# Performance work log

Hardware: AMD Instinct MI355X
Metric: run time of the kernel (lower is better)

The kernel has to match this reference:

```python
import jax, jax.numpy as jnp
import numpy as np

EMBED_DIM = 1024
HEADS = 16
HEAD_DIM = EMBED_DIM // HEADS
ROPE_THETA = 10000.0


def apply_rope(x):
    # x: [B, H, T, D]; standard rotary embedding on head_dim, half-split style
    D = x.shape[-1]
    T = x.shape[-2]
    half = D // 2
    inv_freq = 1.0 / (ROPE_THETA ** (jnp.arange(half, dtype=jnp.float32) / half))
    ang = jnp.arange(T, dtype=jnp.float32)[:, None] * inv_freq[None, :]  # [T, half]
    cos, sin = jnp.cos(ang), jnp.sin(ang)  # [T, half]
    x1, x2 = x[..., :half], x[..., half:]
    return jnp.concatenate([x1 * cos - x2 * sin, x1 * sin + x2 * cos], axis=-1)


def setup_inputs() -> dict:
    key = jax.random.key(0)
    ks = jax.random.split(key, 6)
    B, T, E, H = 2, 2048, EMBED_DIM, HEADS
    s = 0.02
    return {
        "x": jax.random.normal(ks[0], (B, T, E), dtype=jnp.float32),
        "w_qkv": jax.random.normal(ks[1], (E, 3 * E), dtype=jnp.float32) * s,
        "w_pre": jax.random.normal(ks[2], (H, H), dtype=jnp.float32) * s,
        "w_post": jax.random.normal(ks[3], (H, H), dtype=jnp.float32) * s,
        "w_out": jax.random.normal(ks[4], (E, E), dtype=jnp.float32) * s,
        "b_out": jax.random.normal(ks[5], (E,), dtype=jnp.float32) * s,
    }


def reference(x, w_qkv, w_pre, w_post, w_out, b_out):
    B, T, E = x.shape
    H, D = HEADS, HEAD_DIM
    qkv = x @ w_qkv  # [B, T, 3E]
    q, k, v = jnp.split(qkv, 3, axis=-1)
    q = q.reshape(B, T, H, D).transpose(0, 2, 1, 3)  # [B,H,T,D]
    k = k.reshape(B, T, H, D).transpose(0, 2, 1, 3)
    v = v.reshape(B, T, H, D).transpose(0, 2, 1, 3)
    q = apply_rope(q)
    k = apply_rope(k)
    scale = D ** -0.5
    dots = jnp.einsum('bhid,bhjd->bhij', q, k) * scale  # [B,H,T,T]
    # pre-softmax talking-heads mixing: new_head g = sum_h w_pre[g,h] * dots[h]
    dots = jnp.einsum('bhij,gh->bgij', dots, w_pre)
    attn = jax.nn.softmax(dots, axis=-1)
    # post-softmax mixing
    attn = jnp.einsum('bhij,gh->bgij', attn, w_post)
    out = jnp.einsum('bhij,bhjd->bhid', attn, v)  # [B,H,T,D]
    out = out.transpose(0, 2, 1, 3).reshape(B, T, E)
    return out @ w_out.T + b_out  # dropout is identity in eval
```

## Files before the change

### kernel.cpp

```cpp
#include <hip/hip_runtime.h>
#include <stdint.h>

typedef unsigned short u16;
typedef unsigned int   u32;

#define T_SEQ 2048
#define NB 2
#define NH 16
#define HD 64
#define E_DIM 1024
#define E3 3072
#define JS1 4
#define JS2 4
#define S2 36
#define OS2 1040

typedef float f32x4 __attribute__((ext_vector_type(4)));
typedef short s16x8 __attribute__((ext_vector_type(8)));

__device__ __forceinline__ float b2f(u16 u) {
    union { float f; u32 i; } v; v.i = ((u32)u) << 16; return v.f;
}
__device__ __forceinline__ u16 f2b(float f) {
    union { float f; u32 i; } v; v.f = f;
    u32 x = v.i;
    return (u16)((x + 0x7FFFu + ((x >> 16) & 1u)) >> 16);
}
__device__ __forceinline__ f32x4 mfma_bf16(s16x8 a, s16x8 b, f32x4 c) {
    return __builtin_amdgcn_mfma_f32_16x16x32_bf16(a, b, c, 0, 0, 0);
}
__device__ __forceinline__ void gl_lds16(const void* g, void* l) {
    __builtin_amdgcn_global_load_lds((const __attribute__((address_space(1))) void*)g,
                                     (__attribute__((address_space(3))) void*)l, 16, 0, 0);
}

__global__ void k_detect(const u16* __restrict__ x, int* __restrict__ flag) {
    __shared__ int cnt[256];
    int tid = threadIdx.x;
    int insane = 0;
    for (int i = tid; i < 4096; i += 256) {
        u16 v = x[2 * i];
        int e = (v >> 7) & 0xFF;
        if (e >= 143 || (e > 0 && e <= 100)) insane++;
    }
    cnt[tid] = insane;
    __syncthreads();
    if (tid == 0) {
        int s = 0;
        for (int k = 0; k < 256; ++k) s += cnt[k];
        *flag = (s > 512) ? 1 : 0;
    }
}

__global__ void k_cvt_bf16(const void* __restrict__ src, u16* __restrict__ dst,
                           int n, const int* __restrict__ flag) {
    int i = blockIdx.x * 256 + threadIdx.x;
    bool f32 = (*flag) != 0;
    if (i < n) dst[i] = f32 ? f2b(((const float*)src)[i]) : ((const u16*)src)[i];
}

__global__ void k_cvt_small(const void* __restrict__ a, const void* __restrict__ b,
                            const void* __restrict__ c, float* __restrict__ da,
                            float* __restrict__ db, float* __restrict__ dc,
                            const int* __restrict__ flag) {
    int i = blockIdx.x * 256 + threadIdx.x;
    bool f32 = (*flag) != 0;
    if (i < 256) {
        da[i] = f32 ? ((const float*)a)[i] : b2f(((const u16*)a)[i]);
    } else if (i < 512) {
        int j = i - 256;
        db[j] = f32 ? ((const float*)b)[j] : b2f(((const u16*)b)[j]);
    } else if (i < 1536) {
        int j = i - 512;
        dc[j] = f32 ? ((const float*)c)[j] : b2f(((const u16*)c)[j]);
    }
}

__global__ void k_zero(uint4* p, int n16) {
    int i = blockIdx.x * 256 + threadIdx.x;
    if (i < n16) p[i] = uint4{0u, 0u, 0u, 0u};
}

__global__ void k_transpose(const void* __restrict__ w, u16* __restrict__ wT,
                            const int* __restrict__ flag) {
    __shared__ u16 tile[32][33];
    bool f32 = (*flag) != 0;
    int n0 = blockIdx.x * 32;
    int k0 = blockIdx.y * 32;
    int tid = threadIdx.x;
    int c = tid & 31, r4 = tid >> 5;
#pragma unroll
    for (int it = 0; it < 4; ++it) {
        int r = r4 + it * 8;
        size_t idx = (size_t)(k0 + r) * E3 + n0 + c;
        tile[r][c] = f32 ? f2b(((const float*)w)[idx]) : ((const u16*)w)[idx];
    }
    __syncthreads();
#pragma unroll
    for (int it = 0; it < 4; ++it) {
        int r = r4 + it * 8;
        wT[(size_t)(n0 + r) * E_DIM + k0 + c] = tile[c][r];
    }
}

__global__ void k_qkv(const u16* __restrict__ A, const u16* __restrict__ Bm,
                      u16* __restrict__ C) {
    __shared__ __align__(16) u16 As[128 * 32];
    __shared__ __align__(16) u16 Bs[128 * 32];
    int m0 = blockIdx.x * 128, n0 = blockIdx.y * 128;
    int tid = threadIdx.x, lane = tid & 63, wv = tid >> 6;
    int q = lane >> 4, l = lane & 15;
    int wm = (wv >> 1) * 64, wn = (wv & 1) * 64;
    f32x4 acc[4][4] = {};
    int r16 = lane >> 2;
    int ccol = (lane & 3) * 8;
    for (int kc = 0; kc < 1024; kc += 32) {
#pragma unroll
        for (int j = 0; j < 4; ++j) {
            int chunk = wv * 4 + j;
            if (chunk < 8) {
                const u16* g = A + (size_t)(m0 + chunk * 16 + r16) * 1024 + kc + ccol;
                gl_lds16(g, (char*)As + chunk * 1024);
            } else {
                int ch = chunk - 8;
                const u16* g = Bm + (size_t)(n0 + ch * 16 + r16) * 1024 + kc + ccol;
                gl_lds16(g, (char*)Bs + ch * 1024);
            }
        }
        __syncthreads();
        s16x8 af[4], bf[4];
#pragma unroll
        for (int t = 0; t < 4; ++t) {
            af[t] = *(const s16x8*)(As + (wm + t * 16 + l) * 32 + q * 8);
            bf[t] = *(const s16x8*)(Bs + (wn + t * 16 + l) * 32 + q * 8);
        }
#pragma unroll
        for (int i = 0; i < 4; ++i)
#pragma unroll
            for (int j2 = 0; j2 < 4; ++j2)
                acc[i][j2] = mfma_bf16(af[i], bf[j2], acc[i][j2]);
        __syncthreads();
    }
#pragma unroll
    for (int i = 0; i < 4; ++i)
#pragma unroll
        for (int j2 = 0; j2 < 4; ++j2)
#pragma unroll
            for (int r = 0; r < 4; ++r) {
                int row = m0 + wm + i * 16 + q * 4 + r;
                int col = n0 + wn + j2 * 16 + l;
                C[(size_t)row * E3 + col] = f2b(acc[i][j2][r]);
            }
}

__global__ void k_rope(const u16* __restrict__ qkv, u16* __restrict__ qr,
                       u16* __restrict__ kr, u16* __restrict__ vt) {
    __shared__ u16 tile[64][66];
    int t0 = blockIdx.x * 64;
    int h = blockIdx.y, b = blockIdx.z;
    int tid = threadIdx.x;
    const float LN_TH = 9.210340371976184f / 32.0f;
    for (int src = 0; src < 3; ++src) {
        {
            int d = tid & 63, tr = tid >> 6;
#pragma unroll
            for (int it = 0; it < 16; ++it) {
                int t = tr + it * 4;
                tile[t][d] = qkv[(size_t)(b * T_SEQ + t0 + t) * E3 + src * E_DIM + h * HD + d];
            }
        }
        __syncthreads();
        if (src < 2) {
            u16* dst = (src == 0 ? qr : kr) + ((size_t)(b * NH + h) * T_SEQ) * HD;
            int d = tid & 31, tr = tid >> 5;
            float inv = __expf(-(float)d * LN_TH);
#pragma unroll
            for (int it = 0; it < 8; ++it) {
                int t = tr + it * 8;
                float ang = (float)(t0 + t) * inv;
                float sn, cs;
                __sincosf(ang, &sn, &cs);
                float x1 = b2f(tile[t][d]);
                float x2 = b2f(tile[t][d + 32]);
                dst[(size_t)(t0 + t) * HD + d]      = f2b(x1 * cs - x2 * sn);
                dst[(size_t)(t0 + t) * HD + d + 32] = f2b(x1 * sn + x2 * cs);
            }
        } else {
            int tl = tid & 63, dr = tid >> 6;
#pragma unroll
            for (int it = 0; it < 16; ++it) {
                int d = dr + it * 4;
                vt[((size_t)(b * NH + h) * HD + d) * T_SEQ + t0 + tl] = tile[tl][d];
            }
        }
        __syncthreads();
    }
}

__global__ __launch_bounds__(256, 3) void k_pass1(const u16* __restrict__ qr, const u16* __restrict__ kr,
                                                  const float* __restrict__ w_pre, float* __restrict__ lsum) {
    __shared__ __align__(16) u16 dots[256 * S2];
    int lin = blockIdx.x;
    int combo = lin & 7;
    int b = combo >> 2, js = combo & 3;
    int i0 = (lin >> 3) * 32;
    int tid = threadIdx.x, lane = tid & 63, wv = tid >> 6;
    int q = lane >> 4, l = lane & 15;
    {
        uint2* p = (uint2*)(dots + tid * S2 + 16);
        uint2 z = {0u, 0u};
        p[0] = z; p[1] = z; p[2] = z; p[3] = z;
    }
    s16x8 wpre;
#pragma unroll
    for (int jj = 0; jj < 8; ++jj) {
        int hh = q * 8 + jj;
        wpre[jj] = (hh < 16) ? (short)f2b(w_pre[l * 16 + hh] * 0.125f) : (short)0;
    }
    s16x8 qf[2][4][2];
#pragma unroll
    for (int it = 0; it < 2; ++it)
#pragma unroll
        for (int hl = 0; hl < 4; ++hl) {
            int h = wv * 4 + hl;
            const u16* ptr = qr + ((size_t)(b * NH + h) * T_SEQ + i0 + it * 16 + l) * HD + q * 8;
            qf[it][hl][0] = *(const s16x8*)(ptr);
            qf[it][hl][1] = *(const s16x8*)(ptr + 32);
        }
    float lacc[2][4][4] = {};
    __syncthreads();
    int jbase = js * (T_SEQ / JS1);
    for (int jstep = 0; jstep < (T_SEQ / JS1) / 16; ++jstep) {
        int jh = jbase + jstep * 16;
        s16x8 kf[4][2];
#pragma unroll
        for (int hl = 0; hl < 4; ++hl) {
            int h = wv * 4 + hl;
            const u16* ptr = kr + ((size_t)(b * NH + h) * T_SEQ + jh + l) * HD + q * 8;
            kf[hl][0] = *(const s16x8*)(ptr);
            kf[hl][1] = *(const s16x8*)(ptr + 32);
        }
#pragma unroll
        for (int it = 0; it < 2; ++it) {
            f32x4 dacc[4];
#pragma unroll
            for (int hl = 0; hl < 4; ++hl) {
                f32x4 z = {};
                z = mfma_bf16(qf[it][hl][0], kf[hl][0], z);
                z = mfma_bf16(qf[it][hl][1], kf[hl][1], z);
                dacc[hl] = z;
            }
#pragma unroll
            for (int r = 0; r < 4; ++r) {
                int row = (q * 4 + r) * 16 + l;
                uint2 pk;
                pk.x = (u32)f2b(dacc[0][r]) | ((u32)f2b(dacc[1][r]) << 16);
                pk.y = (u32)f2b(dacc[2][r]) | ((u32)f2b(dacc[3][r]) << 16);
                *(uint2*)(dots + row * S2 + wv * 4) = pk;
            }
            __syncthreads();
#pragma unroll
            for (int cl = 0; cl < 4; ++cl) {
                int c = wv * 4 + cl;
                int rbase = (c * 16 + l) * S2;
                union { uint2 u2[2]; s16x8 v; } bf_;
                bf_.u2[0] = *(const uint2*)(dots + rbase + q * 8);
                bf_.u2[1] = *(const uint2*)(dots + rbase + q * 8 + 4);
                f32x4 s = {};
                s = mfma_bf16(wpre, bf_.v, s);
#pragma unroll
                for (int r = 0; r < 4; ++r)
                    lacc[it][cl][r] += __expf(fminf(s[r], 60.0f));
            }
            __syncthreads();
        }
    }
#pragma unroll
    for (int it = 0; it < 2; ++it)
#pragma unroll
        for (int cl = 0; cl < 4; ++cl)
#pragma unroll
            for (int r = 0; r < 4; ++r) {
                float pv = lacc[it][cl][r];
                pv += __shfl_xor(pv, 1);
                pv += __shfl_xor(pv, 2);
                pv += __shfl_xor(pv, 4);
                pv += __shfl_xor(pv, 8);
                if (l == 0) {
                    int g = q * 4 + r;
                    int irow = wv * 4 + cl;
                    atomicAdd(&lsum[(size_t)(b * NH + g) * T_SEQ + i0 + it * 16 + irow], pv);
                }
            }
}

__global__ __launch_bounds__(256, 2) void k_pass2(const u16* __restrict__ qr, const u16* __restrict__ kr,
                                                  const u16* __restrict__ vt, const float* __restrict__ lsum,
                                                  const float* __restrict__ w_pre, const float* __restrict__ w_post,
                                                  u16* __restrict__ opart) {
    __shared__ __align__(16) u16 smem[3 * 256 * S2];
    __shared__ float linv[2][16][16];
    u16* dots = smem;
    u16* aTb  = smem + 256 * S2;
    int lin = blockIdx.x;
    int combo = lin & 7;
    int b = combo >> 2, js = combo & 3;
    int i0 = (lin >> 3) * 32;
    int tid = threadIdx.x, lane = tid & 63, wv = tid >> 6;
    int q = lane >> 4, l = lane & 15;
    {
        uint2* p = (uint2*)(dots + tid * S2 + 16);
        uint2 z = {0u, 0u};
        p[0] = z; p[1] = z; p[2] = z; p[3] = z;
    }
    {
        int g = tid >> 4, il = tid & 15;
        linv[0][g][il] = 1.0f / lsum[(size_t)(b * NH + g) * T_SEQ + i0 + il];
        linv[1][g][il] = 1.0f / lsum[(size_t)(b * NH + g) * T_SEQ + i0 + 16 + il];
    }
    s16x8 wpre, wpost;
#pragma unroll
    for (int jj = 0; jj < 8; ++jj) {
        int hh = q * 8 + jj;
        wpre[jj]  = (hh < 16) ? (short)f2b(w_pre[l * 16 + hh] * 0.125f) : (short)0;
        wpost[jj] = (hh < 16) ? (short)f2b(w_post[l * 16 + hh]) : (short)0;
    }
    s16x8 qf[2][4][2];
#pragma unroll
    for (int it = 0; it < 2; ++it)
#pragma unroll
        for (int hl = 0; hl < 4; ++hl) {
            int h = wv * 4 + hl;
            const u16* ptr = qr + ((size_t)(b * NH + h) * T_SEQ + i0 + it * 16 + l) * HD + q * 8;
            qf[it][hl][0] = *(const s16x8*)(ptr);
            qf[it][hl][1] = *(const s16x8*)(ptr + 32);
        }
    f32x4 oacc[2][4][4] = {};
    __syncthreads();
    int jbase = js * (T_SEQ / JS2);
    for (int jst = 0; jst < (T_SEQ / JS2) / 32; ++jst) {
        int j0 = jbase + jst * 32;
#pragma unroll
        for (int jb = 0; jb < 2; ++jb) {
            int jh = j0 + jb * 16;
            s16x8 kf[4][2];
#pragma unroll
            for (int hl = 0; hl < 4; ++hl) {
                int h = wv * 4 + hl;
                const u16* ptr = kr + ((size_t)(b * NH + h) * T_SEQ + jh + l) * HD + q * 8;
                kf[hl][0] = *(const s16x8*)(ptr);
                kf[hl][1] = *(const s16x8*)(ptr + 32);
            }
#pragma unroll
            for (int it = 0; it < 2; ++it) {
                f32x4 dacc[4];
#pragma unroll
                for (int hl = 0; hl < 4; ++hl) {
                    f32x4 z = {};
                    z = mfma_bf16(qf[it][hl][0], kf[hl][0], z);
                    z = mfma_bf16(qf[it][hl][1], kf[hl][1], z);
                    dacc[hl] = z;
                }
#pragma unroll
                for (int r = 0; r < 4; ++r) {
                    int row = (q * 4 + r) * 16 + l;
                    uint2 pk;
                    pk.x = (u32)f2b(dacc[0][r]) | ((u32)f2b(dacc[1][r]) << 16);
                    pk.y = (u32)f2b(dacc[2][r]) | ((u32)f2b(dacc[3][r]) << 16);
                    *(uint2*)(dots + row * S2 + wv * 4) = pk;
                }
                __syncthreads();
                u16* aT = aTb + it * 256 * S2;
#pragma unroll
                for (int cl = 0; cl < 4; ++cl) {
                    int c = wv * 4 + cl;
                    int rbase = (c * 16 + l) * S2;
                    union { uint2 u2[2]; s16x8 v; } bf_;
                    bf_.u2[0] = *(const uint2*)(dots + rbase + q * 8);
                    bf_.u2[1] = *(const uint2*)(dots + rbase + q * 8 + 4);
                    f32x4 s = {};
                    s = mfma_bf16(wpre, bf_.v, s);
                    u32 pkx, pky;
                    {
                        u16 pu[4];
#pragma unroll
                        for (int r = 0; r < 4; ++r)
                            pu[r] = f2b(__expf(fminf(s[r], 60.0f)) * linv[it][q * 4 + r][c]);
                        pkx = (u32)pu[0] | ((u32)pu[1] << 16);
                        pky = (u32)pu[2] | ((u32)pu[3] << 16);
                    }
                    int srcA = (q & 1) * 32 + l;
                    int srcB = srcA + 16;
                    u32 x0 = (u32)__shfl((int)pkx, srcA);
                    u32 x1 = (u32)__shfl((int)pky, srcA);
                    u32 x2 = (u32)__shfl((int)pkx, srcB);
                    u32 x3 = (u32)__shfl((int)pky, srcB);
                    union { u32 u[4]; s16x8 v; } pf_;
                    bool hi = (q >= 2);
                    pf_.u[0] = hi ? 0u : x0;
                    pf_.u[1] = hi ? 0u : x1;
                    pf_.u[2] = hi ? 0u : x2;
                    pf_.u[3] = hi ? 0u : x3;
                    f32x4 a = {};
                    a = mfma_bf16(wpost, pf_.v, a);
#pragma unroll
                    for (int r = 0; r < 4; ++r)
                        aT[((q * 4 + r) * 16 + c) * S2 + jb * 16 + l] = f2b(a[r]);
                }
                __syncthreads();
            }
        }
#pragma unroll
        for (int gl = 0; gl < 4; ++gl) {
            int gp = wv * 4 + gl;
            int ar = (gp * 16 + l) * S2;
            union { uint2 u2[2]; s16x8 v; } af0, af1;
            af0.u2[0] = *(const uint2*)(aTb + ar + q * 8);
            af0.u2[1] = *(const uint2*)(aTb + ar + q * 8 + 4);
            af1.u2[0] = *(const uint2*)(aTb + 256 * S2 + ar + q * 8);
            af1.u2[1] = *(const uint2*)(aTb + 256 * S2 + ar + q * 8 + 4);
            const u16* vp = vt + ((size_t)(b * NH + gp) * HD) * T_SEQ + j0 + q * 8;
#pragma unroll
            for (int dt = 0; dt < 4; ++dt) {
                s16x8 bfrag = *(const s16x8*)(vp + (size_t)(dt * 16 + l) * T_SEQ);
                oacc[0][gl][dt] = mfma_bf16(af0.v, bfrag, oacc[0][gl][dt]);
                oacc[1][gl][dt] = mfma_bf16(af1.v, bfrag, oacc[1][gl][dt]);
            }
        }
    }
    size_t obase = (size_t)js * ((size_t)NB * T_SEQ * E_DIM);
#pragma unroll
    for (int it = 0; it < 2; ++it) {
        __syncthreads();
        u16* ostage = smem;
#pragma unroll
        for (int gl = 0; gl < 4; ++gl) {
            int gp = wv * 4 + gl;
#pragma unroll
            for (int dt = 0; dt < 4; ++dt)
#pragma unroll
                for (int r = 0; r < 4; ++r)
                    ostage[(q * 4 + r) * OS2 + gp * 64 + dt * 16 + l] = f2b(oacc[it][gl][dt][r]);
        }
        __syncthreads();
        int row = tid >> 4, sl = tid & 15;
        u16* gbase = opart + obase + ((size_t)(b * T_SEQ) + i0 + it * 16 + row) * E_DIM;
#pragma unroll
        for (int w = 0; w < 8; ++w) {
            uint4 v = *(const uint4*)(ostage + row * OS2 + w * 128 + sl * 8);
            *(uint4*)(gbase + w * 128 + sl * 8) = v;
        }
    }
}

__global__ void k_sum(const u16* __restrict__ op, u16* __restrict__ ab) {
    int i = (blockIdx.x * 256 + threadIdx.x) * 8;
    const size_t SZ = (size_t)4096 * 1024;
    union { uint4 v; u16 h[8]; } a0, a1, a2, a3, r;
    a0.v = *(const uint4*)(op + i);
    a1.v = *(const uint4*)(op + SZ + i);
    a2.v = *(const uint4*)(op + 2 * SZ + i);
    a3.v = *(const uint4*)(op + 3 * SZ + i);
#pragma unroll
    for (int k = 0; k < 8; ++k)
        r.h[k] = f2b(b2f(a0.h[k]) + b2f(a1.h[k]) + b2f(a2.h[k]) + b2f(a3.h[k]));
    *(uint4*)(ab + i) = r.v;
}

__global__ void k_outproj(const u16* __restrict__ A, const u16* __restrict__ Bm,
                          const float* __restrict__ bias, void* __restrict__ outv,
                          const int* __restrict__ flag) {
    __shared__ __align__(16) u16 As[128 * 32];
    __shared__ __align__(16) u16 Bs[128 * 32];
    bool f32 = (*flag) != 0;
    int m0 = blockIdx.x * 128, n0 = blockIdx.y * 128;
    int tid = threadIdx.x, lane = tid & 63, wv = tid >> 6;
    int q = lane >> 4, l = lane & 15;
    int wm = (wv >> 1) * 64, wn = (wv & 1) * 64;
    f32x4 acc[4][4] = {};
    int r16 = lane >> 2;
    int ccol = (lane & 3) * 8;
    for (int kc = 0; kc < 1024; kc += 32) {
#pragma unroll
        for (int j = 0; j < 4; ++j) {
            int chunk = wv * 4 + j;
            if (chunk < 8) {
                const u16* g = A + (size_t)(m0 + chunk * 16 + r16) * 1024 + kc + ccol;
                gl_lds16(g, (char*)As + chunk * 1024);
            } else {
                int ch = chunk - 8;
                const u16* g = Bm + (size_t)(n0 + ch * 16 + r16) * 1024 + kc + ccol;
                gl_lds16(g, (char*)Bs + ch * 1024);
            }
        }
        __syncthreads();
        s16x8 af[4], bf[4];
#pragma unroll
        for (int t = 0; t < 4; ++t) {
            af[t] = *(const s16x8*)(As + (wm + t * 16 + l) * 32 + q * 8);
            bf[t] = *(const s16x8*)(Bs + (wn + t * 16 + l) * 32 + q * 8);
        }
#pragma unroll
        for (int i = 0; i < 4; ++i)
#pragma unroll
            for (int j2 = 0; j2 < 4; ++j2)
                acc[i][j2] = mfma_bf16(af[i], bf[j2], acc[i][j2]);
        __syncthreads();
    }
#pragma unroll
    for (int i = 0; i < 4; ++i)
#pragma unroll
        for (int j2 = 0; j2 < 4; ++j2)
#pragma unroll
            for (int r = 0; r < 4; ++r) {
                int row = m0 + wm + i * 16 + q * 4 + r;
                int col = n0 + wn + j2 * 16 + l;
                float val = acc[i][j2][r] + bias[col];
                size_t idx = (size_t)row * E_DIM + col;
                if (f32) ((float*)outv)[idx] = val;
                else     ((u16*)outv)[idx]   = f2b(val);
            }
}

extern "C" void kernel_launch(void* const* d_in, const int* in_sizes, int n_in,
                              void* d_out, int out_size, void* d_ws, size_t ws_size,
                              hipStream_t stream) {
    (void)in_sizes; (void)n_in; (void)out_size; (void)ws_size;
    const void* x      = d_in[0];
    const void* w_qkv  = d_in[1];
    const void* w_pre  = d_in[2];
    const void* w_post = d_in[3];
    const void* w_out  = d_in[4];
    const void* b_out  = d_in[5];

    char* ws = (char*)d_ws;
    size_t off = 0;
    auto alloc = [&](size_t bytes) -> char* {
        char* p = ws + off;
        off += (bytes + 255) & ~(size_t)255;
        return p;
    };
    char* region0 = alloc((size_t)(8 + 6 + 24) * 1024 * 1024);
    u16*  xb      = (u16*)region0;
    u16*  wqkvT   = (u16*)(region0 + (size_t)8 * 1024 * 1024);
    u16*  qkv     = (u16*)(region0 + (size_t)14 * 1024 * 1024);
    u16*  opart   = (u16*)region0;
    int*  flag    = (int*)alloc(256);
    u16*  woutb   = (u16*)alloc((size_t)1024 * 1024 * 2);
    float* wpre_c = (float*)alloc(256 * 4);
    float* wpost_c= (float*)alloc(256 * 4);
    float* bout_c = (float*)alloc(1024 * 4);
    u16*  qr      = (u16*)alloc((size_t)NB * NH * T_SEQ * HD * 2);
    u16*  kr      = (u16*)alloc((size_t)NB * NH * T_SEQ * HD * 2);
    u16*  vt      = (u16*)alloc((size_t)NB * NH * HD * T_SEQ * 2);
    float* lsum   = (float*)alloc((size_t)NB * NH * T_SEQ * 4);
    u16*  ab      = (u16*)alloc((size_t)4096 * 1024 * 2);

    k_detect<<<1, 256, 0, stream>>>((const u16*)x, flag);
    k_cvt_bf16<<<16384, 256, 0, stream>>>(x, xb, 4096 * 1024, flag);
    k_cvt_bf16<<<4096, 256, 0, stream>>>(w_out, woutb, 1024 * 1024, flag);
    k_cvt_small<<<6, 256, 0, stream>>>(w_pre, w_post, b_out, wpre_c, wpost_c, bout_c, flag);
    {
        int n16 = (int)(((size_t)NB * NH * T_SEQ * 4) / 16);
        k_zero<<<(n16 + 255) / 256, 256, 0, stream>>>((uint4*)lsum, n16);
    }
    k_transpose<<<dim3(96, 32), 256, 0, stream>>>(w_qkv, wqkvT, flag);
    k_qkv<<<dim3(32, 24), 256, 0, stream>>>(xb, wqkvT, qkv);
    k_rope<<<dim3(32, 16, 2), 256, 0, stream>>>(qkv, qr, kr, vt);
    k_pass1<<<512, 256, 0, stream>>>(qr, kr, wpre_c, lsum);
    k_pass2<<<512, 256, 0, stream>>>(qr, kr, vt, lsum, wpre_c, wpost_c, opart);
    k_sum<<<2048, 256, 0, stream>>>(opart, ab);
    k_outproj<<<dim3(32, 8), 256, 0, stream>>>(ab, woutb, bout_c, d_out, flag);
}
```

Measured before the change: 536.8 us.

## Double-buffer dots LDS tile to drop barriers; replace lsum atomics with partials

The dots scratch buffer in pass1 and pass2 becomes two alternating LDS buffers. This lets the second __syncthreads per sub-iteration be removed in pass1, and in pass2 the per-iteration barrier is moved to a single barrier before the PV product. The atomicAdd accumulation of softmax denominators is replaced by per-split partial writes that pass2 sums itself, which also removes the zeroing kernel. The cost is more LDS per block in pass2 (4 buffers instead of 3), which may reduce occupancy. The barrier removal also depends on buffer reuse distance being safe, which is a race risk.

Result: slower. 574.2 us (+7.0%).

```diff
diff --git a/kernel.cpp b/kernel.cpp
--- a/kernel.cpp
+++ b/kernel.cpp
@@ -76,11 +76,6 @@
     }
 }
 
-__global__ void k_zero(uint4* p, int n16) {
-    int i = blockIdx.x * 256 + threadIdx.x;
-    if (i < n16) p[i] = uint4{0u, 0u, 0u, 0u};
-}
-
 __global__ void k_transpose(const void* __restrict__ w, u16* __restrict__ wT,
                             const int* __restrict__ flag) {
     __shared__ u16 tile[32][33];
@@ -198,8 +193,8 @@
 }
 
 __global__ __launch_bounds__(256, 3) void k_pass1(const u16* __restrict__ qr, const u16* __restrict__ kr,
-                                                  const float* __restrict__ w_pre, float* __restrict__ lsum) {
-    __shared__ __align__(16) u16 dots[256 * S2];
+                                                  const float* __restrict__ w_pre, float* __restrict__ lpart) {
+    __shared__ __align__(16) u16 dotsb[2 * 256 * S2];
     int lin = blockIdx.x;
     int combo = lin & 7;
     int b = combo >> 2, js = combo & 3;
@@ -207,9 +202,11 @@
     int tid = threadIdx.x, lane = tid & 63, wv = tid >> 6;
     int q = lane >> 4, l = lane & 15;
     {
-        uint2* p = (uint2*)(dots + tid * S2 + 16);
         uint2 z = {0u, 0u};
-        p[0] = z; p[1] = z; p[2] = z; p[3] = z;
+        uint2* p0 = (uint2*)(dotsb + tid * S2 + 16);
+        uint2* p1 = (uint2*)(dotsb + 256 * S2 + tid * S2 + 16);
+        p0[0] = z; p0[1] = z; p0[2] = z; p0[3] = z;
+        p1[0] = z; p1[1] = z; p1[2] = z; p1[3] = z;
     }
     s16x8 wpre;
 #pragma unroll
@@ -242,6 +239,7 @@
         }
 #pragma unroll
         for (int it = 0; it < 2; ++it) {
+            u16* dots = dotsb + (it & 1) * 256 * S2;
             f32x4 dacc[4];
 #pragma unroll
             for (int hl = 0; hl < 4; ++hl) {
@@ -272,7 +270,6 @@
                 for (int r = 0; r < 4; ++r)
                     lacc[it][cl][r] += __expf(fminf(s[r], 60.0f));
             }
-            __syncthreads();
         }
     }
 #pragma unroll
@@ -289,19 +286,19 @@
                 if (l == 0) {
                     int g = q * 4 + r;
                     int irow = wv * 4 + cl;
-                    atomicAdd(&lsum[(size_t)(b * NH + g) * T_SEQ + i0 + it * 16 + irow], pv);
+                    lpart[((size_t)(combo * NH + g)) * T_SEQ + i0 + it * 16 + irow] = pv;
                 }
             }
 }
 
 __global__ __launch_bounds__(256, 2) void k_pass2(const u16* __restrict__ qr, const u16* __restrict__ kr,
-                                                  const u16* __restrict__ vt, const float* __restrict__ lsum,
+                                                  const u16* __restrict__ vt, const float* __restrict__ lpart,
                                                   const float* __restrict__ w_pre, const float* __restrict__ w_post,
                                                   u16* __restrict__ opart) {
-    __shared__ __align__(16) u16 smem[3 * 256 * S2];
+    __shared__ __align__(16) u16 smem[4 * 256 * S2];
     __shared__ float linv[2][16][16];
-    u16* dots = smem;
-    u16* aTb  = smem + 256 * S2;
+    u16* dotsb = smem;
+    u16* aTb   = smem + 2 * 256 * S2;
     int lin = blockIdx.x;
     int combo = lin & 7;
     int b = combo >> 2, js = combo & 3;
@@ -309,14 +306,23 @@
     int tid = threadIdx.x, lane = tid & 63, wv = tid >> 6;
     int q = lane >> 4, l = lane & 15;
     {
-        uint2* p = (uint2*)(dots + tid * S2 + 16);
         uint2 z = {0u, 0u};
-        p[0] = z; p[1] = z; p[2] = z; p[3] = z;
+        uint2* p0 = (uint2*)(dotsb + tid * S2 + 16);
+        uint2* p1 = (uint2*)(dotsb + 256 * S2 + tid * S2 + 16);
+        p0[0] = z; p0[1] = z; p0[2] = z; p0[3] = z;
+        p1[0] = z; p1[1] = z; p1[2] = z; p1[3] = z;
     }
     {
         int g = tid >> 4, il = tid & 15;
-        linv[0][g][il] = 1.0f / lsum[(size_t)(b * NH + g) * T_SEQ + i0 + il];
-        linv[1][g][il] = 1.0f / lsum[(size_t)(b * NH + g) * T_SEQ + i0 + 16 + il];
+        float s0 = 0.f, s1 = 0.f;
+#pragma unroll
+        for (int j4 = 0; j4 < 4; ++j4) {
+            const float* lp = lpart + ((size_t)((b * 4 + j4) * NH + g)) * T_SEQ + i0;
+            s0 += lp[il];
+            s1 += lp[16 + il];
+        }
+        linv[0][g][il] = 1.0f / s0;
+        linv[1][g][il] = 1.0f / s1;
     }
     s16x8 wpre, wpost;
 #pragma unroll
@@ -353,6 +359,7 @@
             }
 #pragma unroll
             for (int it = 0; it < 2; ++it) {
+                u16* dots = dotsb + ((jb * 2 + it) & 1) * 256 * S2;
                 f32x4 dacc[4];
 #pragma unroll
                 for (int hl = 0; hl < 4; ++hl) {
@@ -407,9 +414,9 @@
                     for (int r = 0; r < 4; ++r)
                         aT[((q * 4 + r) * 16 + c) * S2 + jb * 16 + l] = f2b(a[r]);
                 }
-                __syncthreads();
-            }
-        }
+            }
+        }
+        __syncthreads();
 #pragma unroll
         for (int gl = 0; gl < 4; ++gl) {
             int gp = wv * 4 + gl;
@@ -553,22 +560,18 @@
     u16*  qr      = (u16*)alloc((size_t)NB * NH * T_SEQ * HD * 2);
     u16*  kr      = (u16*)alloc((size_t)NB * NH * T_SEQ * HD * 2);
     u16*  vt      = (u16*)alloc((size_t)NB * NH * HD * T_SEQ * 2);
-    float* lsum   = (float*)alloc((size_t)NB * NH * T_SEQ * 4);
+    float* lpart  = (float*)alloc((size_t)8 * NH * T_SEQ * 4);
     u16*  ab      = (u16*)alloc((size_t)4096 * 1024 * 2);
 
     k_detect<<<1, 256, 0, stream>>>((const u16*)x, flag);
     k_cvt_bf16<<<16384, 256, 0, stream>>>(x, xb, 4096 * 1024, flag);
     k_cvt_bf16<<<4096, 256, 0, stream>>>(w_out, woutb, 1024 * 1024, flag);
     k_cvt_small<<<6, 256, 0, stream>>>(w_pre, w_post, b_out, wpre_c, wpost_c, bout_c, flag);
-    {
-        int n16 = (int)(((size_t)NB * NH * T_SEQ * 4) / 16);
-        k_zero<<<(n16 + 255) / 256, 256, 0, stream>>>((uint4*)lsum, n16);
-    }
     k_transpose<<<dim3(96, 32), 256, 0, stream>>>(w_qkv, wqkvT, flag);
     k_qkv<<<dim3(32, 24), 256, 0, stream>>>(xb, wqkvT, qkv);
     k_rope<<<dim3(32, 16, 2), 256, 0, stream>>>(qkv, qr, kr, vt);
-    k_pass1<<<512, 256, 0, stream>>>(qr, kr, wpre_c, lsum);
-    k_pass2<<<512, 256, 0, stream>>>(qr, kr, vt, lsum, wpre_c, wpost_c, opart);
+    k_pass1<<<512, 256, 0, stream>>>(qr, kr, wpre_c, lpart);
+    k_pass2<<<512, 256, 0, stream>>>(qr, kr, vt, lpart, wpre_c, wpost_c, opart);
     k_sum<<<2048, 256, 0, stream>>>(opart, ab);
     k_outproj<<<dim3(32, 8), 256, 0, stream>>>(ab, woutb, bout_c, d_out, flag);
 }
```
